# Performance work log

Measured on AMD Instinct MI355X. Metric: run time of the kernel, lower is better.

The kernel has to match this reference:

```python
import jax, jax.numpy as jnp
import numpy as np

# ---- reconstructed Constants (repo's Constants module is external) ----
DT, DX, DY, Z = 0.005, 0.01, 0.01, 1.0
_cf = np.array([-11.0 / 6.0, 3.0, -1.5, 1.0 / 3.0], np.float32)  # 3rd-order one-sided stencil
KF  = jnp.asarray(((DT / DX) * _cf).reshape(1, 4, 1, 1))           # H-field forward boundary kernel
KB  = jnp.asarray((-(DT / DX) * _cf[::-1]).reshape(1, 4, 1, 1))    # H-field backward boundary kernel
KEF = jnp.asarray(((DT / (Z * DY)) * _cf).reshape(1, 4, 1, 1))     # E-field forward boundary kernel
KEB = jnp.asarray((-(DT / (Z * DY)) * _cf[::-1]).reshape(1, 4, 1, 1))

PAD1   = ((0, 0), (2, 2), (2, 2), (0, 0))
PAD2   = ((0, 0), (0, 0), (1, 1), (0, 0))
PAD3   = ((0, 0), (1, 1), (0, 0), (0, 0))
PADY_F = ((0, 0), (0, 4), (1, 1), (0, 0))
PADY_B = ((0, 0), (4, 0), (1, 1), (0, 0))
PADX_F = ((0, 0), (1, 1), (0, 4), (0, 0))
PADX_B = ((0, 0), (1, 1), (4, 0), (0, 0))
PADEX_F = ((0, 0), (0, 0), (0, 2), (0, 0))
PADEX_B = ((0, 0), (0, 0), (2, 0), (0, 0))
PADEY_F = ((0, 0), (0, 2), (0, 0), (0, 0))
PADEY_B = ((0, 0), (2, 0), (0, 0), (0, 0))


def _conv(x, k):  # TF-style VALID cross-correlation, NHWC/HWIO
    return jax.lax.conv_general_dilated(x, k, (1, 1), 'VALID',
                                        dimension_numbers=('NHWC', 'HWIO', 'NHWC'))


def _T(k):  # swap the two spatial kernel dims (tf.transpose perm=[1,0,2,3])
    return jnp.transpose(k, (1, 0, 2, 3))


def _amper(E, Hx, Hy, f):
    S1 = (jnp.pad(DT / DX * _conv(Hy, _T(f)), PAD1)
          + jnp.pad(_conv(Hy, _T(KF)), PADY_F)
          + jnp.pad(_conv(Hy, _T(KB)), PADY_B))
    S2 = (jnp.pad(Z * DT / DY * _conv(Hx, f), PAD1)
          + jnp.pad(_conv(Hx, KF), PADX_F)
          + jnp.pad(_conv(Hx, KB), PADX_B))
    return E + S1 - S2


def _faraday(E, Hx, Hy, f):
    S3 = (DT / (Z * DY) * jnp.pad(_conv(E, f), PAD2)
          + jnp.pad(_conv(E, KEF), PADEX_F)[:, 1:-1, :, :]
          + jnp.pad(_conv(E, KEB), PADEX_B)[:, 1:-1, :, :])
    S4 = (DT / (Z * DX) * jnp.pad(_conv(E, _T(f)), PAD3)
          + jnp.pad(_conv(E, _T(KEF)), PADEY_F)[:, :, 1:-1, :]
          + jnp.pad(_conv(E, _T(KEB)), PADEY_B)[:, :, 1:-1, :])
    return Hx - S3, Hy + S4


def setup_inputs() -> dict:
    key = jax.random.key(0)
    k1, k2, k3 = jax.random.split(key, 3)
    B, P, Q = 8, 1024, 1024
    E = jax.random.normal(k1, (B, P, Q, 1), jnp.float32)
    Hx = jax.random.normal(k2, (B, P - 2, Q - 1, 1), jnp.float32)
    Hy = jax.random.normal(k3, (B, P - 1, Q - 2, 1), jnp.float32)
    filt = jnp.array([[1.0, -1.0, 1.0, 0.0],
                      [0.0, -1.0, 1.0, 0.0],
                      [1.0, -1.0, 1.0, 0.0]], jnp.float32).reshape(3, 4, 1, 1)
    return {'E': E, 'Hx': Hx, 'Hy': Hy, 'filt': filt}


def reference(E, Hx, Hy, filt):
    E_n = _amper(E, Hx, Hy, filt)
    Hx_n, Hy_n = _faraday(E_n, Hx, Hy, filt)
    E_m = _amper(E_n, Hx_n, Hy_n, filt)
    Hx_m, Hy_m = _faraday(E_m, Hx_n, Hy_n, filt)
    return (jnp.concatenate([E_n, E_m], 1),
            jnp.concatenate([Hx_n, Hx_m], 1),
            jnp.concatenate([Hy_n, Hy_m], 1))
```

## Files before the change

kernel.cpp:

```cpp
#include <hip/hip_runtime.h>


#define KF0 (-11.0f / 12.0f)
#define KF1 (1.5f)
#define KF2 (-0.75f)
#define KF3 (1.0f / 6.0f)
#define KB0 (-1.0f / 6.0f)
#define KB1 (0.75f)
#define KB2 (-1.5f)
#define KB3 (11.0f / 12.0f)

__global__ __launch_bounds__(256) void amper_k(
    const float* __restrict__ E, int sEb,
    const float* __restrict__ Hx, int sHxb,
    const float* __restrict__ Hy, int sHyb,
    float* __restrict__ Eo, int sEob)
{
    int x = blockIdx.x * 256 + threadIdx.x;
    int y = blockIdx.y;
    int b = blockIdx.z;
    const float* e  = E  + (size_t)b * sEb;
    const float* hx = Hx + (size_t)b * sHxb;
    const float* hy = Hy + (size_t)b * sHyb;

    float v = e[y * 1024 + x];

    if ((y >= 2) & (y < 1022) & (x >= 2) & (x < 1022)) {
        const float* r0 = hy + (y - 2) * 1022 + (x - 2);
        const float* r1 = r0 + 1022;
        const float* r2 = r1 + 1022;
        v += 0.5f * ((r0[0] + r0[2])
                     - (r1[0] + r1[1] + r1[2])
                     + (r2[0] + r2[1] + r2[2]));
        const float* q0 = hx + (y - 2) * 1023 + (x - 2);
        const float* q1 = q0 + 1023;
        const float* q2 = q1 + 1023;
        v -= 0.5f * ((q0[0] - q0[1] + q0[2])
                     + (-q1[1] + q1[2])
                     + (q2[0] - q2[1] + q2[2]));
    }
    bool cx = (x >= 1) & (x < 1023);
    if ((y < 1020) & cx) {
        const float* c = hy + y * 1022 + (x - 1);
        v += KF0 * c[0] + KF1 * c[1022] + KF2 * c[2044] + KF3 * c[3066];
    }
    if ((y >= 4) & cx) {
        const float* c = hy + (y - 4) * 1022 + (x - 1);
        v += KB0 * c[0] + KB1 * c[1022] + KB2 * c[2044] + KB3 * c[3066];
    }
    bool cy = (y >= 1) & (y < 1023);
    if (cy & (x < 1020)) {
        const float* r = hx + (y - 1) * 1023 + x;
        v -= KF0 * r[0] + KF1 * r[1] + KF2 * r[2] + KF3 * r[3];
    }
    if (cy & (x >= 4)) {
        const float* r = hx + (y - 1) * 1023 + (x - 4);
        v -= KB0 * r[0] + KB1 * r[1] + KB2 * r[2] + KB3 * r[3];
    }

    Eo[(size_t)b * sEob + y * 1024 + x] = v;
}

__global__ __launch_bounds__(256) void faraday_k(
    const float* __restrict__ E, int sEb,
    const float* __restrict__ Hx, int sHxb,
    const float* __restrict__ Hy, int sHyb,
    float* __restrict__ Hxo, int sHxob,
    float* __restrict__ Hyo, int sHyob)
{
    int x = blockIdx.x * 256 + threadIdx.x;
    int y = blockIdx.y;
    int b = blockIdx.z;
    const float* e = E + (size_t)b * sEb;

    if ((x < 1023) & (y < 1022)) {
        float v = (Hx + (size_t)b * sHxb)[y * 1023 + x];
        if ((x >= 1) & (x < 1022)) {
            const float* r0 = e + y * 1024 + (x - 1);
            const float* r1 = r0 + 1024;
            const float* r2 = r1 + 1024;
            v -= 0.5f * ((r0[0] - r0[1] + r0[2])
                         + (-r1[1] + r1[2])
                         + (r2[0] - r2[1] + r2[2]));
        }
        if (x < 1021) {
            const float* r = e + (y + 1) * 1024 + x;
            v -= KF0 * r[0] + KF1 * r[1] + KF2 * r[2] + KF3 * r[3];
        }
        if (x >= 2) {
            const float* r = e + (y + 1) * 1024 + (x - 2);
            v -= KB0 * r[0] + KB1 * r[1] + KB2 * r[2] + KB3 * r[3];
        }
        Hxo[(size_t)b * sHxob + y * 1023 + x] = v;
    }

    if (x < 1022) {
        float v = (Hy + (size_t)b * sHyb)[y * 1022 + x];
        if ((y >= 1) & (y < 1022)) {
            const float* r0 = e + (y - 1) * 1024 + x;
            const float* r1 = r0 + 1024;
            const float* r2 = r1 + 1024;
            v += 0.5f * ((r0[0] + r0[2])
                         - (r1[0] + r1[1] + r1[2])
                         + (r2[0] + r2[1] + r2[2]));
        }
        if (y < 1021) {
            const float* c = e + y * 1024 + (x + 1);
            v += KF0 * c[0] + KF1 * c[1024] + KF2 * c[2048] + KF3 * c[3072];
        }
        if (y >= 2) {
            const float* c = e + (y - 2) * 1024 + (x + 1);
            v += KB0 * c[0] + KB1 * c[1024] + KB2 * c[2048] + KB3 * c[3072];
        }
        Hyo[(size_t)b * sHyob + y * 1022 + x] = v;
    }
}

extern "C" void kernel_launch(void* const* d_in, const int* in_sizes, int n_in,
                              void* d_out, int out_size, void* d_ws, size_t ws_size,
                              hipStream_t stream)
{
    const float* E  = (const float*)d_in[0];
    const float* Hx = (const float*)d_in[1];
    const float* Hy = (const float*)d_in[2];

    float* out = (float*)d_out;
    float* Eo  = out;
    float* Hxo = out + 16777216;
    float* Hyo = Hxo + 16728096;

    const int sE = 1024 * 1024;
    const int sHx = 1022 * 1023;
    const int sHy = 1023 * 1022;
    const int sEo = 2 * 1024 * 1024;
    const int sHo = 2 * 1045506;

    dim3 blk(256, 1, 1);
    dim3 gA(4, 1024, 8);
    dim3 gF(4, 1023, 8);

    amper_k<<<gA, blk, 0, stream>>>(E, sE, Hx, sHx, Hy, sHy, Eo, sEo);
    faraday_k<<<gF, blk, 0, stream>>>(Eo, sEo, Hx, sHx, Hy, sHy,
                                      Hxo, sHo, Hyo, sHo);
    amper_k<<<gA, blk, 0, stream>>>(Eo, sEo, Hxo, sHo, Hyo, sHo,
                                    Eo + 1024 * 1024, sEo);
    faraday_k<<<gF, blk, 0, stream>>>(Eo + 1024 * 1024, sEo, Hxo, sHo, Hyo, sHo,
                                      Hxo + 1045506, sHo, Hyo + 1045506, sHo);
}
```

Measured before the change: 444.3 us.

## Compute four outputs per thread with vectorized row loads and register reuse

Each thread now computes four consecutive outputs. Interior points load their stencil rows as float4/float2 vectors and reuse overlapping values in registers, while boundary points fall back to scalar per-point helpers. Block indices are remapped so consecutive blocks interleave the batch index. This cuts the number of load instructions and redundant global reads, but many of the vector loads are unaligned (odd row strides such as 1022 and 1023) and the grid has a quarter as many threads.

```diff
diff --git a/kernel.cpp b/kernel.cpp
--- a/kernel.cpp
+++ b/kernel.cpp
@@ -10,21 +10,25 @@
 #define KB2 (-1.5f)
 #define KB3 (11.0f / 12.0f)
 
-__global__ __launch_bounds__(256) void amper_k(
-    const float* __restrict__ E, int sEb,
-    const float* __restrict__ Hx, int sHxb,
-    const float* __restrict__ Hy, int sHyb,
-    float* __restrict__ Eo, int sEob)
-{
-    int x = blockIdx.x * 256 + threadIdx.x;
-    int y = blockIdx.y;
-    int b = blockIdx.z;
-    const float* e  = E  + (size_t)b * sEb;
-    const float* hx = Hx + (size_t)b * sHxb;
-    const float* hy = Hy + (size_t)b * sHyb;
-
+typedef float f4 __attribute__((ext_vector_type(4)));
+typedef float f2 __attribute__((ext_vector_type(2)));
+
+__device__ __forceinline__ f4 ld4(const float* p) { f4 v; __builtin_memcpy(&v, p, 16); return v; }
+__device__ __forceinline__ f2 ld2(const float* p) { f2 v; __builtin_memcpy(&v, p, 8); return v; }
+__device__ __forceinline__ void st4(float* p, f4 v) { __builtin_memcpy(p, &v, 16); }
+
+#define LOAD6(dst, p) do { f4 _a = ld4(p); f2 _b = ld2((p) + 4); \
+    (dst)[0]=_a.x; (dst)[1]=_a.y; (dst)[2]=_a.z; (dst)[3]=_a.w; (dst)[4]=_b.x; (dst)[5]=_b.y; } while (0)
+#define LOAD4(dst, p) do { f4 _a = ld4(p); \
+    (dst)[0]=_a.x; (dst)[1]=_a.y; (dst)[2]=_a.z; (dst)[3]=_a.w; } while (0)
+
+
+__device__ __forceinline__ float amper_pt(const float* __restrict__ e,
+                                          const float* __restrict__ hx,
+                                          const float* __restrict__ hy,
+                                          int y, int x)
+{
     float v = e[y * 1024 + x];
-
     if ((y >= 2) & (y < 1022) & (x >= 2) & (x < 1022)) {
         const float* r0 = hy + (y - 2) * 1022 + (x - 2);
         const float* r1 = r0 + 1022;
@@ -57,9 +61,120 @@
         const float* r = hx + (y - 1) * 1023 + (x - 4);
         v -= KB0 * r[0] + KB1 * r[1] + KB2 * r[2] + KB3 * r[3];
     }
-
-    Eo[(size_t)b * sEob + y * 1024 + x] = v;
-}
+    return v;
+}
+
+__device__ __forceinline__ float far_hx_pt(const float* __restrict__ e,
+                                           const float* __restrict__ hxp,
+                                           int y, int x)
+{
+    float v = hxp[y * 1023 + x];
+    if ((x >= 1) & (x < 1022)) {
+        const float* r0 = e + y * 1024 + (x - 1);
+        const float* r1 = r0 + 1024;
+        const float* r2 = r1 + 1024;
+        v -= 0.5f * ((r0[0] - r0[1] + r0[2])
+                     + (-r1[1] + r1[2])
+                     + (r2[0] - r2[1] + r2[2]));
+    }
+    if (x < 1021) {
+        const float* r = e + (y + 1) * 1024 + x;
+        v -= KF0 * r[0] + KF1 * r[1] + KF2 * r[2] + KF3 * r[3];
+    }
+    if (x >= 2) {
+        const float* r = e + (y + 1) * 1024 + (x - 2);
+        v -= KB0 * r[0] + KB1 * r[1] + KB2 * r[2] + KB3 * r[3];
+    }
+    return v;
+}
+
+__device__ __forceinline__ float far_hy_pt(const float* __restrict__ e,
+                                           const float* __restrict__ hyp,
+                                           int y, int x)
+{
+    float v = hyp[y * 1022 + x];
+    if ((y >= 1) & (y < 1022)) {
+        const float* r0 = e + (y - 1) * 1024 + x;
+        const float* r1 = r0 + 1024;
+        const float* r2 = r1 + 1024;
+        v += 0.5f * ((r0[0] + r0[2])
+                     - (r1[0] + r1[1] + r1[2])
+                     + (r2[0] + r2[1] + r2[2]));
+    }
+    if (y < 1021) {
+        const float* c = e + y * 1024 + (x + 1);
+        v += KF0 * c[0] + KF1 * c[1024] + KF2 * c[2048] + KF3 * c[3072];
+    }
+    if (y >= 2) {
+        const float* c = e + (y - 2) * 1024 + (x + 1);
+        v += KB0 * c[0] + KB1 * c[1024] + KB2 * c[2048] + KB3 * c[3072];
+    }
+    return v;
+}
+
+
+__global__ __launch_bounds__(256) void amper_k(
+    const float* __restrict__ E, int sEb,
+    const float* __restrict__ Hx, int sHxb,
+    const float* __restrict__ Hy, int sHyb,
+    float* __restrict__ Eo, int sEob)
+{
+    int lin = blockIdx.y + (blockIdx.z << 10);
+    int b = lin & 7;
+    int y = lin >> 3;
+    int x0 = threadIdx.x << 2;
+
+    const float* e  = E  + (size_t)b * sEb;
+    const float* hx = Hx + (size_t)b * sHxb;
+    const float* hy = Hy + (size_t)b * sHyb;
+    float* eo = Eo + (size_t)b * sEob + y * 1024;
+
+    if ((y >= 4) & (y < 1020) & (x0 >= 4) & (x0 <= 1016)) {
+        float cA[6], cB[6], cC[6];
+        const float* hyr = hy + (y - 2) * 1022 + (x0 - 2);
+        LOAD6(cA, hyr);
+        LOAD6(cB, hyr + 1022);
+        LOAD6(cC, hyr + 2044);
+        float km4[4], km3[4], kp1[4], kp2[4], kp3[4];
+        const float* hyc = hy + (y - 4) * 1022 + (x0 - 1);
+        LOAD4(km4, hyc);
+        LOAD4(km3, hyc + 1022);
+        LOAD4(kp1, hyc + 5 * 1022);
+        LOAD4(kp2, hyc + 6 * 1022);
+        LOAD4(kp3, hyc + 7 * 1022);
+        float dA[6], dC[6], e12[12];
+        const float* hxr = hx + (y - 2) * 1023 + (x0 - 2);
+        LOAD6(dA, hxr);
+        LOAD6(dC, hxr + 2046);
+        const float* hxm = hx + (y - 1) * 1023 + (x0 - 4);
+        LOAD4(&e12[0], hxm);
+        LOAD4(&e12[4], hxm + 4);
+        LOAD4(&e12[8], hxm + 8);
+        f4 ev = ld4(e + y * 1024 + x0);
+        f4 o;
+        #pragma unroll
+        for (int j = 0; j < 4; ++j) {
+            float v = ev[j];
+            v += 0.5f * ((cA[j] + cA[j + 2])
+                         - (cB[j] + cB[j + 1] + cB[j + 2])
+                         + (cC[j] + cC[j + 1] + cC[j + 2]));
+            v -= 0.5f * ((dA[j] - dA[j + 1] + dA[j + 2])
+                         + (-e12[j + 3] + e12[j + 4])
+                         + (dC[j] - dC[j + 1] + dC[j + 2]));
+            v += KF0 * cC[j + 1] + KF1 * kp1[j] + KF2 * kp2[j] + KF3 * kp3[j];
+            v += KB0 * km4[j] + KB1 * km3[j] + KB2 * cA[j + 1] + KB3 * cB[j + 1];
+            v -= KF0 * e12[j + 4] + KF1 * e12[j + 5] + KF2 * e12[j + 6] + KF3 * e12[j + 7];
+            v -= KB0 * e12[j] + KB1 * e12[j + 1] + KB2 * e12[j + 2] + KB3 * e12[j + 3];
+            o[j] = v;
+        }
+        st4(eo + x0, o);
+    } else {
+        #pragma unroll
+        for (int j = 0; j < 4; ++j)
+            eo[x0 + j] = amper_pt(e, hx, hy, y, x0 + j);
+    }
+}
+
 
 __global__ __launch_bounds__(256) void faraday_k(
     const float* __restrict__ E, int sEb,
@@ -68,51 +183,79 @@
     float* __restrict__ Hxo, int sHxob,
     float* __restrict__ Hyo, int sHyob)
 {
-    int x = blockIdx.x * 256 + threadIdx.x;
-    int y = blockIdx.y;
-    int b = blockIdx.z;
+    int lin = blockIdx.y + 1023 * blockIdx.z;
+    int b = lin & 7;
+    int y = lin >> 3;
+    int x0 = threadIdx.x << 2;
+
     const float* e = E + (size_t)b * sEb;
-
-    if ((x < 1023) & (y < 1022)) {
-        float v = (Hx + (size_t)b * sHxb)[y * 1023 + x];
-        if ((x >= 1) & (x < 1022)) {
-            const float* r0 = e + y * 1024 + (x - 1);
-            const float* r1 = r0 + 1024;
-            const float* r2 = r1 + 1024;
-            v -= 0.5f * ((r0[0] - r0[1] + r0[2])
-                         + (-r1[1] + r1[2])
-                         + (r2[0] - r2[1] + r2[2]));
+    bool xfast = (x0 >= 4) & (x0 <= 1016);
+
+    if (y < 1022) {
+        const float* hxp = Hx + (size_t)b * sHxb;
+        float* hxo = Hxo + (size_t)b * sHxob + y * 1023;
+        if (xfast) {
+            float gA[6], gC[6], h9[9];
+            const float* er = e + y * 1024 + (x0 - 1);
+            LOAD6(gA, er);
+            LOAD6(gC, er + 2048);
+            const float* em = e + (y + 1) * 1024 + (x0 - 2);
+            LOAD4(&h9[0], em);
+            LOAD4(&h9[4], em + 4);
+            h9[8] = em[8];
+            f4 hv = ld4(hxp + y * 1023 + x0);
+            f4 o;
+            #pragma unroll
+            for (int j = 0; j < 4; ++j) {
+                float v = hv[j];
+                v -= 0.5f * ((gA[j] - gA[j + 1] + gA[j + 2])
+                             + (-h9[j + 2] + h9[j + 3])
+                             + (gC[j] - gC[j + 1] + gC[j + 2]));
+                v -= KF0 * h9[j + 2] + KF1 * h9[j + 3] + KF2 * h9[j + 4] + KF3 * h9[j + 5];
+                v -= KB0 * h9[j] + KB1 * h9[j + 1] + KB2 * h9[j + 2] + KB3 * h9[j + 3];
+                o[j] = v;
+            }
+            st4(hxo + x0, o);
+        } else {
+            for (int j = 0; j < 4; ++j) {
+                int x = x0 + j;
+                if (x < 1023) hxo[x] = far_hx_pt(e, hxp, y, x);
+            }
         }
-        if (x < 1021) {
-            const float* r = e + (y + 1) * 1024 + x;
-            v -= KF0 * r[0] + KF1 * r[1] + KF2 * r[2] + KF3 * r[3];
+    }
+
+    {
+        const float* hyp = Hy + (size_t)b * sHyb;
+        float* hyo = Hyo + (size_t)b * sHyob + y * 1022;
+        if (xfast & (y >= 2) & (y <= 1020)) {
+            float mA[6], mB[6], mC[6], nA[4], nD[4], nE[4];
+            const float* er = e + (y - 1) * 1024 + x0;
+            LOAD6(mA, er);
+            LOAD6(mB, er + 1024);
+            LOAD6(mC, er + 2048);
+            const float* en = e + (y - 2) * 1024 + (x0 + 1);
+            LOAD4(nA, en);
+            LOAD4(nD, en + 4 * 1024);
+            LOAD4(nE, en + 5 * 1024);
+            f4 hv = ld4(hyp + y * 1022 + x0);
+            f4 o;
+            #pragma unroll
+            for (int j = 0; j < 4; ++j) {
+                float v = hv[j];
+                v += 0.5f * ((mA[j] + mA[j + 2])
+                             - (mB[j] + mB[j + 1] + mB[j + 2])
+                             + (mC[j] + mC[j + 1] + mC[j + 2]));
+                v += KF0 * mB[j + 1] + KF1 * mC[j + 1] + KF2 * nD[j] + KF3 * nE[j];
+                v += KB0 * nA[j] + KB1 * mA[j + 1] + KB2 * mB[j + 1] + KB3 * mC[j + 1];
+                o[j] = v;
+            }
+            st4(hyo + x0, o);
+        } else {
+            for (int j = 0; j < 4; ++j) {
+                int x = x0 + j;
+                if (x < 1022) hyo[x] = far_hy_pt(e, hyp, y, x);
+            }
         }
-        if (x >= 2) {
-            const float* r = e + (y + 1) * 1024 + (x - 2);
-            v -= KB0 * r[0] + KB1 * r[1] + KB2 * r[2] + KB3 * r[3];
-        }
-        Hxo[(size_t)b * sHxob + y * 1023 + x] = v;
-    }
-
-    if (x < 1022) {
-        float v = (Hy + (size_t)b * sHyb)[y * 1022 + x];
-        if ((y >= 1) & (y < 1022)) {
-            const float* r0 = e + (y - 1) * 1024 + x;
-            const float* r1 = r0 + 1024;
-            const float* r2 = r1 + 1024;
-            v += 0.5f * ((r0[0] + r0[2])
-                         - (r1[0] + r1[1] + r1[2])
-                         + (r2[0] + r2[1] + r2[2]));
-        }
-        if (y < 1021) {
-            const float* c = e + y * 1024 + (x + 1);
-            v += KF0 * c[0] + KF1 * c[1024] + KF2 * c[2048] + KF3 * c[3072];
-        }
-        if (y >= 2) {
-            const float* c = e + (y - 2) * 1024 + (x + 1);
-            v += KB0 * c[0] + KB1 * c[1024] + KB2 * c[2048] + KB3 * c[3072];
-        }
-        Hyo[(size_t)b * sHyob + y * 1022 + x] = v;
     }
 }
 
@@ -136,8 +279,8 @@
     const int sHo = 2 * 1045506;
 
     dim3 blk(256, 1, 1);
-    dim3 gA(4, 1024, 8);
-    dim3 gF(4, 1023, 8);
+    dim3 gA(1, 1024, 8);
+    dim3 gF(1, 1023, 8);
 
     amper_k<<<gA, blk, 0, stream>>>(E, sE, Hx, sHx, Hy, sHy, Eo, sEo);
     faraday_k<<<gF, blk, 0, stream>>>(Eo, sEo, Hx, sHx, Hy, sHy,
```

Result: faster. 400.5 us (-9.9%).

## Fuse amper and faraday steps via LDS-staged E tile with halo recompute

Applied to the files above, without the earlier changes.

Merges the amper and faraday kernels into one kernel per half-step. Each block computes the updated E for an 8-row by 512-column tile plus halo rows and columns, keeps it in shared memory, and writes the interior to global memory. It then computes the Hx and Hy updates directly from shared memory. Interior work is vectorized to four elements per thread using 16-byte loads and stores. This removes the global write-then-reread of E between kernels and halves the launch count, at the cost of recomputing halo rows (13 rows per 8 output rows) and only 256 blocks per launch.

```diff
diff --git a/kernel.cpp b/kernel.cpp
--- a/kernel.cpp
+++ b/kernel.cpp
@@ -10,21 +10,20 @@
 #define KB2 (-1.5f)
 #define KB3 (11.0f / 12.0f)
 
-__global__ __launch_bounds__(256) void amper_k(
-    const float* __restrict__ E, int sEb,
-    const float* __restrict__ Hx, int sHxb,
-    const float* __restrict__ Hy, int sHyb,
-    float* __restrict__ Eo, int sEob)
-{
-    int x = blockIdx.x * 256 + threadIdx.x;
-    int y = blockIdx.y;
-    int b = blockIdx.z;
-    const float* e  = E  + (size_t)b * sEb;
-    const float* hx = Hx + (size_t)b * sHxb;
-    const float* hy = Hy + (size_t)b * sHyb;
-
+typedef float f4 __attribute__((ext_vector_type(4)));
+
+__device__ __forceinline__ f4 ld4(const float* p) { f4 v; __builtin_memcpy(&v, p, 16); return v; }
+__device__ __forceinline__ void st4(float* p, f4 v) { __builtin_memcpy(p, &v, 16); }
+
+#define LOAD6(dst, p) do { __builtin_memcpy(dst, p, 24); } while (0)
+#define LOAD4(dst, p) do { __builtin_memcpy(dst, p, 16); } while (0)
+
+__device__ __forceinline__ float amper_pt(const float* __restrict__ e,
+                                          const float* __restrict__ hx,
+                                          const float* __restrict__ hy,
+                                          int y, int x)
+{
     float v = e[y * 1024 + x];
-
     if ((y >= 2) & (y < 1022) & (x >= 2) & (x < 1022)) {
         const float* r0 = hy + (y - 2) * 1022 + (x - 2);
         const float* r1 = r0 + 1022;
@@ -57,62 +56,210 @@
         const float* r = hx + (y - 1) * 1023 + (x - 4);
         v -= KB0 * r[0] + KB1 * r[1] + KB2 * r[2] + KB3 * r[3];
     }
-
-    Eo[(size_t)b * sEob + y * 1024 + x] = v;
-}
-
-__global__ __launch_bounds__(256) void faraday_k(
+    return v;
+}
+
+#define EP 532
+#define ES_AT(r, c) eS[((r) - y0 + 2) * EP + ((c) - xb + 4)]
+
+__device__ __forceinline__ float far_hx_pt_lds(
+    const float* eS, const float* __restrict__ hxp,
+    int y0, int xb, int y, int x)
+{
+    float v = hxp[y * 1023 + x];
+    if ((x >= 1) & (x < 1022)) {
+        v -= 0.5f * ((ES_AT(y, x-1) - ES_AT(y, x) + ES_AT(y, x+1))
+                     + (-ES_AT(y+1, x) + ES_AT(y+1, x+1))
+                     + (ES_AT(y+2, x-1) - ES_AT(y+2, x) + ES_AT(y+2, x+1)));
+    }
+    if (x < 1021) {
+        v -= KF0 * ES_AT(y+1, x) + KF1 * ES_AT(y+1, x+1)
+           + KF2 * ES_AT(y+1, x+2) + KF3 * ES_AT(y+1, x+3);
+    }
+    if (x >= 2) {
+        v -= KB0 * ES_AT(y+1, x-2) + KB1 * ES_AT(y+1, x-1)
+           + KB2 * ES_AT(y+1, x) + KB3 * ES_AT(y+1, x+1);
+    }
+    return v;
+}
+
+__device__ __forceinline__ float far_hy_pt_lds(
+    const float* eS, const float* __restrict__ hyp,
+    int y0, int xb, int y, int x)
+{
+    float v = hyp[y * 1022 + x];
+    if ((y >= 1) & (y < 1022)) {
+        v += 0.5f * ((ES_AT(y-1, x) + ES_AT(y-1, x+2))
+                     - (ES_AT(y, x) + ES_AT(y, x+1) + ES_AT(y, x+2))
+                     + (ES_AT(y+1, x) + ES_AT(y+1, x+1) + ES_AT(y+1, x+2)));
+    }
+    if (y < 1021) {
+        v += KF0 * ES_AT(y, x+1) + KF1 * ES_AT(y+1, x+1)
+           + KF2 * ES_AT(y+2, x+1) + KF3 * ES_AT(y+3, x+1);
+    }
+    if (y >= 2) {
+        v += KB0 * ES_AT(y-2, x+1) + KB1 * ES_AT(y-1, x+1)
+           + KB2 * ES_AT(y, x+1) + KB3 * ES_AT(y+1, x+1);
+    }
+    return v;
+}
+
+__global__ __launch_bounds__(256) void fused_k(
     const float* __restrict__ E, int sEb,
     const float* __restrict__ Hx, int sHxb,
     const float* __restrict__ Hy, int sHyb,
+    float* __restrict__ Eo, int sEob,
     float* __restrict__ Hxo, int sHxob,
     float* __restrict__ Hyo, int sHyob)
 {
-    int x = blockIdx.x * 256 + threadIdx.x;
-    int y = blockIdx.y;
-    int b = blockIdx.z;
-    const float* e = E + (size_t)b * sEb;
-
-    if ((x < 1023) & (y < 1022)) {
-        float v = (Hx + (size_t)b * sHxb)[y * 1023 + x];
-        if ((x >= 1) & (x < 1022)) {
-            const float* r0 = e + y * 1024 + (x - 1);
-            const float* r1 = r0 + 1024;
-            const float* r2 = r1 + 1024;
-            v -= 0.5f * ((r0[0] - r0[1] + r0[2])
-                         + (-r1[1] + r1[2])
-                         + (r2[0] - r2[1] + r2[2]));
+    int xt = blockIdx.x;
+    int b  = blockIdx.y;
+    int s  = blockIdx.z;
+    int y0 = s << 3;
+    int xb = xt << 9;
+
+    const float* e  = E  + (size_t)b * sEb;
+    const float* hx = Hx + (size_t)b * sHxb;
+    const float* hy = Hy + (size_t)b * sHyb;
+    float* eo  = Eo  + (size_t)b * sEob;
+    float* hxo = Hxo + (size_t)b * sHxob;
+    float* hyo = Hyo + (size_t)b * sHyob;
+
+    __shared__ float eS[13 * EP];
+
+    int tid = threadIdx.x;
+
+    for (int idx = tid; idx < 13 * 132; idx += 256) {
+        int i = idx / 132, j = idx - i * 132;
+        int y  = y0 - 2 + i;
+        int c0 = xb - 4 + (j << 2);
+        if ((unsigned)y < 1024u) {
+            f4 o;
+            if ((y >= 4) & (y < 1020) & (c0 >= 4) & (c0 <= 1016)) {
+                float cA[6], cB[6], cC[6];
+                const float* hyr = hy + (y - 2) * 1022 + (c0 - 2);
+                LOAD6(cA, hyr);
+                LOAD6(cB, hyr + 1022);
+                LOAD6(cC, hyr + 2044);
+                float km4[4], km3[4], kp1[4], kp2[4], kp3[4];
+                const float* hyc = hy + (y - 4) * 1022 + (c0 - 1);
+                LOAD4(km4, hyc);
+                LOAD4(km3, hyc + 1022);
+                LOAD4(kp1, hyc + 5 * 1022);
+                LOAD4(kp2, hyc + 6 * 1022);
+                LOAD4(kp3, hyc + 7 * 1022);
+                float dA[6], dC[6], e12[12];
+                const float* hxr = hx + (y - 2) * 1023 + (c0 - 2);
+                LOAD6(dA, hxr);
+                LOAD6(dC, hxr + 2046);
+                const float* hxm = hx + (y - 1) * 1023 + (c0 - 4);
+                LOAD4(&e12[0], hxm);
+                LOAD4(&e12[4], hxm + 4);
+                LOAD4(&e12[8], hxm + 8);
+                f4 ev = ld4(e + y * 1024 + c0);
+                #pragma unroll
+                for (int k = 0; k < 4; ++k) {
+                    float v = ev[k];
+                    v += 0.5f * ((cA[k] + cA[k + 2])
+                                 - (cB[k] + cB[k + 1] + cB[k + 2])
+                                 + (cC[k] + cC[k + 1] + cC[k + 2]));
+                    v -= 0.5f * ((dA[k] - dA[k + 1] + dA[k + 2])
+                                 + (-e12[k + 3] + e12[k + 4])
+                                 + (dC[k] - dC[k + 1] + dC[k + 2]));
+                    v += KF0 * cC[k + 1] + KF1 * kp1[k] + KF2 * kp2[k] + KF3 * kp3[k];
+                    v += KB0 * km4[k] + KB1 * km3[k] + KB2 * cA[k + 1] + KB3 * cB[k + 1];
+                    v -= KF0 * e12[k + 4] + KF1 * e12[k + 5] + KF2 * e12[k + 6] + KF3 * e12[k + 7];
+                    v -= KB0 * e12[k] + KB1 * e12[k + 1] + KB2 * e12[k + 2] + KB3 * e12[k + 3];
+                    o[k] = v;
+                }
+            } else {
+                #pragma unroll
+                for (int k = 0; k < 4; ++k) {
+                    int x = c0 + k;
+                    o[k] = ((unsigned)x < 1024u) ? amper_pt(e, hx, hy, y, x) : 0.f;
+                }
+            }
+            st4(&eS[i * EP + (c0 - xb + 4)], o);
+            if ((y >= y0) & (y < y0 + 8) & (c0 >= xb) & (c0 <= xb + 508))
+                st4(eo + y * 1024 + c0, o);
         }
-        if (x < 1021) {
-            const float* r = e + (y + 1) * 1024 + x;
-            v -= KF0 * r[0] + KF1 * r[1] + KF2 * r[2] + KF3 * r[3];
+    }
+    __syncthreads();
+
+    int tx = tid & 127, ty = tid >> 7;
+    int c0 = xb + (tx << 2);
+    bool cfast = (c0 >= 4) & (c0 <= 1016);
+
+    #pragma unroll
+    for (int rr = 0; rr < 4; ++rr) {
+        int y = y0 + (ty << 2) + rr;
+
+        if (y < 1022) {
+            float* hxorow = hxo + y * 1023;
+            if (cfast) {
+                const float* er = &eS[(y - y0 + 2) * EP + (c0 - xb + 3)];
+                float gA[6], gC[6], h9[9];
+                LOAD6(gA, er);
+                LOAD6(gC, er + 2 * EP);
+                const float* em = &eS[(y - y0 + 3) * EP + (c0 - xb + 2)];
+                LOAD4(&h9[0], em);
+                LOAD4(&h9[4], em + 4);
+                h9[8] = em[8];
+                f4 hv = ld4(hx + y * 1023 + c0);
+                f4 o;
+                #pragma unroll
+                for (int k = 0; k < 4; ++k) {
+                    float v = hv[k];
+                    v -= 0.5f * ((gA[k] - gA[k + 1] + gA[k + 2])
+                                 + (-h9[k + 2] + h9[k + 3])
+                                 + (gC[k] - gC[k + 1] + gC[k + 2]));
+                    v -= KF0 * h9[k + 2] + KF1 * h9[k + 3] + KF2 * h9[k + 4] + KF3 * h9[k + 5];
+                    v -= KB0 * h9[k] + KB1 * h9[k + 1] + KB2 * h9[k + 2] + KB3 * h9[k + 3];
+                    o[k] = v;
+                }
+                st4(hxorow + c0, o);
+            } else {
+                #pragma unroll
+                for (int k = 0; k < 4; ++k) {
+                    int x = c0 + k;
+                    if (x < 1023) hxorow[x] = far_hx_pt_lds(eS, hx, y0, xb, y, x);
+                }
+            }
         }
-        if (x >= 2) {
-            const float* r = e + (y + 1) * 1024 + (x - 2);
-            v -= KB0 * r[0] + KB1 * r[1] + KB2 * r[2] + KB3 * r[3];
+
+        if (y < 1023) {
+            float* hyorow = hyo + y * 1022;
+            if (cfast & (y >= 2) & (y <= 1020)) {
+                const float* er = &eS[(y - y0 + 1) * EP + (c0 - xb + 4)];
+                float mA[6], mB[6], mC[6], nA[4], nD[4], nE[4];
+                LOAD6(mA, er);
+                LOAD6(mB, er + EP);
+                LOAD6(mC, er + 2 * EP);
+                const float* en = &eS[(y - y0) * EP + (c0 - xb + 5)];
+                LOAD4(nA, en);
+                LOAD4(nD, en + 4 * EP);
+                LOAD4(nE, en + 5 * EP);
+                f4 hv = ld4(hy + y * 1022 + c0);
+                f4 o;
+                #pragma unroll
+                for (int k = 0; k < 4; ++k) {
+                    float v = hv[k];
+                    v += 0.5f * ((mA[k] + mA[k + 2])
+                                 - (mB[k] + mB[k + 1] + mB[k + 2])
+                                 + (mC[k] + mC[k + 1] + mC[k + 2]));
+                    v += KF0 * mB[k + 1] + KF1 * mC[k + 1] + KF2 * nD[k] + KF3 * nE[k];
+                    v += KB0 * nA[k] + KB1 * mA[k + 1] + KB2 * mB[k + 1] + KB3 * mC[k + 1];
+                    o[k] = v;
+                }
+                st4(hyorow + c0, o);
+            } else {
+                #pragma unroll
+                for (int k = 0; k < 4; ++k) {
+                    int x = c0 + k;
+                    if (x < 1022) hyorow[x] = far_hy_pt_lds(eS, hy, y0, xb, y, x);
+                }
+            }
         }
-        Hxo[(size_t)b * sHxob + y * 1023 + x] = v;
-    }
-
-    if (x < 1022) {
-        float v = (Hy + (size_t)b * sHyb)[y * 1022 + x];
-        if ((y >= 1) & (y < 1022)) {
-            const float* r0 = e + (y - 1) * 1024 + x;
-            const float* r1 = r0 + 1024;
-            const float* r2 = r1 + 1024;
-            v += 0.5f * ((r0[0] + r0[2])
-                         - (r1[0] + r1[1] + r1[2])
-                         + (r2[0] + r2[1] + r2[2]));
-        }
-        if (y < 1021) {
-            const float* c = e + y * 1024 + (x + 1);
-            v += KF0 * c[0] + KF1 * c[1024] + KF2 * c[2048] + KF3 * c[3072];
-        }
-        if (y >= 2) {
-            const float* c = e + (y - 2) * 1024 + (x + 1);
-            v += KB0 * c[0] + KB1 * c[1024] + KB2 * c[2048] + KB3 * c[3072];
-        }
-        Hyo[(size_t)b * sHyob + y * 1022 + x] = v;
     }
 }
 
@@ -129,21 +276,18 @@
     float* Hxo = out + 16777216;
     float* Hyo = Hxo + 16728096;
 
-    const int sE = 1024 * 1024;
+    const int sE  = 1024 * 1024;
     const int sHx = 1022 * 1023;
     const int sHy = 1023 * 1022;
     const int sEo = 2 * 1024 * 1024;
     const int sHo = 2 * 1045506;
 
     dim3 blk(256, 1, 1);
-    dim3 gA(4, 1024, 8);
-    dim3 gF(4, 1023, 8);
-
-    amper_k<<<gA, blk, 0, stream>>>(E, sE, Hx, sHx, Hy, sHy, Eo, sEo);
-    faraday_k<<<gF, blk, 0, stream>>>(Eo, sEo, Hx, sHx, Hy, sHy,
-                                      Hxo, sHo, Hyo, sHo);
-    amper_k<<<gA, blk, 0, stream>>>(Eo, sEo, Hxo, sHo, Hyo, sHo,
-                                    Eo + 1024 * 1024, sEo);
-    faraday_k<<<gF, blk, 0, stream>>>(Eo + 1024 * 1024, sEo, Hxo, sHo, Hyo, sHo,
-                                      Hxo + 1045506, sHo, Hyo + 1045506, sHo);
-}
+    dim3 g(2, 8, 128);
+
+    fused_k<<<g, blk, 0, stream>>>(E, sE, Hx, sHx, Hy, sHy,
+                                   Eo, sEo, Hxo, sHo, Hyo, sHo);
+    fused_k<<<g, blk, 0, stream>>>(Eo, sEo, Hxo, sHo, Hyo, sHo,
+                                   Eo + 1024 * 1024, sEo,
+                                   Hxo + 1045506, sHo, Hyo + 1045506, sHo);
+}
```

Result: slower. 516.3 us (+16.2%).

## Register-tile stencils: 4 columns x 8 rows per thread with rolling row windows

Applied to the files above, without the earlier changes.

Both stencil kernels are restructured so each thread produces 4 adjacent columns over 8 consecutive rows. Input rows are held in a rolling register window, so each loaded row serves several output rows. Loads and stores become wider vector accesses, and edge columns go through a scalar fallback path. This cuts redundant global and L2 loads and per-element index arithmetic, at the cost of far fewer blocks (1024 per launch), higher register pressure, and possibly misaligned vector accesses on the 1023- and 1022-wide rows.

```diff
diff --git a/kernel.cpp b/kernel.cpp
--- a/kernel.cpp
+++ b/kernel.cpp
@@ -10,21 +10,18 @@
 #define KB2 (-1.5f)
 #define KB3 (11.0f / 12.0f)
 
-__global__ __launch_bounds__(256) void amper_k(
-    const float* __restrict__ E, int sEb,
-    const float* __restrict__ Hx, int sHxb,
-    const float* __restrict__ Hy, int sHyb,
-    float* __restrict__ Eo, int sEob)
-{
-    int x = blockIdx.x * 256 + threadIdx.x;
-    int y = blockIdx.y;
-    int b = blockIdx.z;
-    const float* e  = E  + (size_t)b * sEb;
-    const float* hx = Hx + (size_t)b * sHxb;
-    const float* hy = Hy + (size_t)b * sHyb;
-
+typedef float f4 __attribute__((ext_vector_type(4)));
+
+__device__ __forceinline__ f4 ld4(const float* p) { f4 v; __builtin_memcpy(&v, p, 16); return v; }
+__device__ __forceinline__ void st4(float* p, f4 v) { __builtin_memcpy(p, &v, 16); }
+
+
+__device__ __forceinline__ float amper_pt(const float* __restrict__ e,
+                                          const float* __restrict__ hx,
+                                          const float* __restrict__ hy,
+                                          int y, int x)
+{
     float v = e[y * 1024 + x];
-
     if ((y >= 2) & (y < 1022) & (x >= 2) & (x < 1022)) {
         const float* r0 = hy + (y - 2) * 1022 + (x - 2);
         const float* r1 = r0 + 1022;
@@ -57,62 +54,286 @@
         const float* r = hx + (y - 1) * 1023 + (x - 4);
         v -= KB0 * r[0] + KB1 * r[1] + KB2 * r[2] + KB3 * r[3];
     }
-
-    Eo[(size_t)b * sEob + y * 1024 + x] = v;
-}
-
-__global__ __launch_bounds__(256) void faraday_k(
+    return v;
+}
+
+__device__ __forceinline__ float far_hx_pt(const float* __restrict__ e,
+                                           const float* __restrict__ hxp,
+                                           int y, int x)
+{
+    float v = hxp[y * 1023 + x];
+    if ((x >= 1) & (x < 1022)) {
+        const float* r0 = e + y * 1024 + (x - 1);
+        const float* r1 = r0 + 1024;
+        const float* r2 = r1 + 1024;
+        v -= 0.5f * ((r0[0] - r0[1] + r0[2])
+                     + (-r1[1] + r1[2])
+                     + (r2[0] - r2[1] + r2[2]));
+    }
+    if (x < 1021) {
+        const float* r = e + (y + 1) * 1024 + x;
+        v -= KF0 * r[0] + KF1 * r[1] + KF2 * r[2] + KF3 * r[3];
+    }
+    if (x >= 2) {
+        const float* r = e + (y + 1) * 1024 + (x - 2);
+        v -= KB0 * r[0] + KB1 * r[1] + KB2 * r[2] + KB3 * r[3];
+    }
+    return v;
+}
+
+__device__ __forceinline__ float far_hy_pt(const float* __restrict__ e,
+                                           const float* __restrict__ hyp,
+                                           int y, int x)
+{
+    float v = hyp[y * 1022 + x];
+    if ((y >= 1) & (y < 1022)) {
+        const float* r0 = e + (y - 1) * 1024 + x;
+        const float* r1 = r0 + 1024;
+        const float* r2 = r1 + 1024;
+        v += 0.5f * ((r0[0] + r0[2])
+                     - (r1[0] + r1[1] + r1[2])
+                     + (r2[0] + r2[1] + r2[2]));
+    }
+    if (y < 1021) {
+        const float* c = e + y * 1024 + (x + 1);
+        v += KF0 * c[0] + KF1 * c[1024] + KF2 * c[2048] + KF3 * c[3072];
+    }
+    if (y >= 2) {
+        const float* c = e + (y - 2) * 1024 + (x + 1);
+        v += KB0 * c[0] + KB1 * c[1024] + KB2 * c[2048] + KB3 * c[3072];
+    }
+    return v;
+}
+
+
+__global__ __launch_bounds__(256) void amper_m(
+    const float* __restrict__ E, int sEb,
+    const float* __restrict__ Hx, int sHxb,
+    const float* __restrict__ Hy, int sHyb,
+    float* __restrict__ Eo, int sEob)
+{
+    int b  = blockIdx.x;
+    int y0 = blockIdx.y << 3;
+    int tid = threadIdx.x;
+    int x0 = tid << 2;
+
+    const float* e  = E  + (size_t)b * sEb;
+    const float* hx = Hx + (size_t)b * sHxb;
+    const float* hy = Hy + (size_t)b * sHyb;
+    float* eo = Eo + (size_t)b * sEob;
+
+    bool fast = (x0 >= 4) & (x0 <= 1016);
+
+    if (fast) {
+        float W[8][6];
+        float X[4][12];
+
+        #pragma unroll
+        for (int t = -4; t <= 2; ++t) {
+            int gr = y0 + t;
+            float* w = W[(t + 8) & 7];
+            if ((unsigned)gr < 1023u) {
+                __builtin_memcpy(w, hy + gr * 1022 + (x0 - 2), 24);
+            } else {
+                #pragma unroll
+                for (int k = 0; k < 6; ++k) w[k] = 0.f;
+            }
+        }
+        #pragma unroll
+        for (int t = -2; t <= -1; ++t) {
+            int gr = y0 + t;
+            float* w = X[(t + 8) & 3];
+            if ((unsigned)gr < 1022u) {
+                __builtin_memcpy(w, hx + gr * 1023 + (x0 - 4), 48);
+            } else {
+                #pragma unroll
+                for (int k = 0; k < 12; ++k) w[k] = 0.f;
+            }
+        }
+
+        #define WY(d) (W[(i + (d) + 8) & 7])
+        #define XX(d) (X[(i + (d) + 8) & 3])
+
+        #pragma unroll
+        for (int i = 0; i < 8; ++i) {
+            int y = y0 + i;
+            {
+                int gr = y + 3;
+                float* w = W[(i + 3) & 7];
+                if (gr <= 1022) {
+                    __builtin_memcpy(w, hy + gr * 1022 + (x0 - 2), 24);
+                } else {
+                    #pragma unroll
+                    for (int k = 0; k < 6; ++k) w[k] = 0.f;
+                }
+            }
+            {
+                float* w = X[(i + 8) & 3];
+                if (y <= 1021) {
+                    __builtin_memcpy(w, hx + y * 1023 + (x0 - 4), 48);
+                } else {
+                    #pragma unroll
+                    for (int k = 0; k < 12; ++k) w[k] = 0.f;
+                }
+            }
+            f4 ev = ld4(e + y * 1024 + x0);
+            f4 o;
+            bool gin = (y >= 2) & (y < 1022);
+            bool gf  = (y < 1020);
+            bool gb  = (y >= 4);
+            bool gc  = (y >= 1) & (y < 1023);
+            #pragma unroll
+            for (int j = 0; j < 4; ++j) {
+                float v = ev[j];
+                if (gin) {
+                    v += 0.5f * ((WY(-2)[j] + WY(-2)[j + 2])
+                                 - (WY(-1)[j] + WY(-1)[j + 1] + WY(-1)[j + 2])
+                                 + (WY(0)[j] + WY(0)[j + 1] + WY(0)[j + 2]));
+                    v -= 0.5f * ((XX(-2)[j + 2] - XX(-2)[j + 3] + XX(-2)[j + 4])
+                                 + (-XX(-1)[j + 3] + XX(-1)[j + 4])
+                                 + (XX(0)[j + 2] - XX(0)[j + 3] + XX(0)[j + 4]));
+                }
+                if (gf)
+                    v += KF0 * WY(0)[j + 1] + KF1 * WY(1)[j + 1]
+                       + KF2 * WY(2)[j + 1] + KF3 * WY(3)[j + 1];
+                if (gb)
+                    v += KB0 * WY(-4)[j + 1] + KB1 * WY(-3)[j + 1]
+                       + KB2 * WY(-2)[j + 1] + KB3 * WY(-1)[j + 1];
+                if (gc) {
+                    v -= KF0 * XX(-1)[j + 4] + KF1 * XX(-1)[j + 5]
+                       + KF2 * XX(-1)[j + 6] + KF3 * XX(-1)[j + 7];
+                    v -= KB0 * XX(-1)[j] + KB1 * XX(-1)[j + 1]
+                       + KB2 * XX(-1)[j + 2] + KB3 * XX(-1)[j + 3];
+                }
+                o[j] = v;
+            }
+            st4(eo + y * 1024 + x0, o);
+        }
+        #undef WY
+        #undef XX
+    } else {
+        for (int i = 0; i < 8; ++i) {
+            int y = y0 + i;
+            #pragma unroll
+            for (int k = 0; k < 4; ++k)
+                eo[y * 1024 + x0 + k] = amper_pt(e, hx, hy, y, x0 + k);
+        }
+    }
+}
+
+
+__global__ __launch_bounds__(256) void faraday_m(
     const float* __restrict__ E, int sEb,
     const float* __restrict__ Hx, int sHxb,
     const float* __restrict__ Hy, int sHyb,
     float* __restrict__ Hxo, int sHxob,
     float* __restrict__ Hyo, int sHyob)
 {
-    int x = blockIdx.x * 256 + threadIdx.x;
-    int y = blockIdx.y;
-    int b = blockIdx.z;
-    const float* e = E + (size_t)b * sEb;
-
-    if ((x < 1023) & (y < 1022)) {
-        float v = (Hx + (size_t)b * sHxb)[y * 1023 + x];
-        if ((x >= 1) & (x < 1022)) {
-            const float* r0 = e + y * 1024 + (x - 1);
-            const float* r1 = r0 + 1024;
-            const float* r2 = r1 + 1024;
-            v -= 0.5f * ((r0[0] - r0[1] + r0[2])
-                         + (-r1[1] + r1[2])
-                         + (r2[0] - r2[1] + r2[2]));
-        }
-        if (x < 1021) {
-            const float* r = e + (y + 1) * 1024 + x;
-            v -= KF0 * r[0] + KF1 * r[1] + KF2 * r[2] + KF3 * r[3];
-        }
-        if (x >= 2) {
-            const float* r = e + (y + 1) * 1024 + (x - 2);
-            v -= KB0 * r[0] + KB1 * r[1] + KB2 * r[2] + KB3 * r[3];
-        }
-        Hxo[(size_t)b * sHxob + y * 1023 + x] = v;
-    }
-
-    if (x < 1022) {
-        float v = (Hy + (size_t)b * sHyb)[y * 1022 + x];
-        if ((y >= 1) & (y < 1022)) {
-            const float* r0 = e + (y - 1) * 1024 + x;
-            const float* r1 = r0 + 1024;
-            const float* r2 = r1 + 1024;
-            v += 0.5f * ((r0[0] + r0[2])
-                         - (r1[0] + r1[1] + r1[2])
-                         + (r2[0] + r2[1] + r2[2]));
-        }
-        if (y < 1021) {
-            const float* c = e + y * 1024 + (x + 1);
-            v += KF0 * c[0] + KF1 * c[1024] + KF2 * c[2048] + KF3 * c[3072];
-        }
-        if (y >= 2) {
-            const float* c = e + (y - 2) * 1024 + (x + 1);
-            v += KB0 * c[0] + KB1 * c[1024] + KB2 * c[2048] + KB3 * c[3072];
-        }
-        Hyo[(size_t)b * sHyob + y * 1022 + x] = v;
+    int b  = blockIdx.x;
+    int y0 = blockIdx.y << 3;
+    int tid = threadIdx.x;
+    int x0 = tid << 2;
+
+    const float* e   = E  + (size_t)b * sEb;
+    const float* hxp = Hx + (size_t)b * sHxb;
+    const float* hyp = Hy + (size_t)b * sHyb;
+    float* hxo = Hxo + (size_t)b * sHxob;
+    float* hyo = Hyo + (size_t)b * sHyob;
+
+    bool fast = (x0 >= 4) & (x0 <= 1016);
+
+    if (fast) {
+        float Ew[8][12];
+
+        #pragma unroll
+        for (int t = -2; t <= 2; ++t) {
+            int gr = y0 + t;
+            float* w = Ew[(t + 8) & 7];
+            if ((unsigned)gr < 1024u) {
+                __builtin_memcpy(w, e + gr * 1024 + (x0 - 4), 48);
+            } else {
+                #pragma unroll
+                for (int k = 0; k < 12; ++k) w[k] = 0.f;
+            }
+        }
+
+        #define EWD(d) (Ew[(i + (d) + 8) & 7])
+
+        #pragma unroll
+        for (int i = 0; i < 8; ++i) {
+            int y = y0 + i;
+            {
+                int gr = y + 3;
+                float* w = Ew[(i + 3) & 7];
+                if (gr <= 1023) {
+                    __builtin_memcpy(w, e + gr * 1024 + (x0 - 4), 48);
+                } else {
+                    #pragma unroll
+                    for (int k = 0; k < 12; ++k) w[k] = 0.f;
+                }
+            }
+
+            if (y < 1022) {
+                f4 hv = ld4(hxp + y * 1023 + x0);
+                f4 o;
+                #pragma unroll
+                for (int j = 0; j < 4; ++j) {
+                    float v = hv[j];
+                    v -= 0.5f * ((EWD(0)[j + 3] - EWD(0)[j + 4] + EWD(0)[j + 5])
+                                 + (-EWD(1)[j + 4] + EWD(1)[j + 5])
+                                 + (EWD(2)[j + 3] - EWD(2)[j + 4] + EWD(2)[j + 5]));
+                    v -= KF0 * EWD(1)[j + 4] + KF1 * EWD(1)[j + 5]
+                       + KF2 * EWD(1)[j + 6] + KF3 * EWD(1)[j + 7];
+                    v -= KB0 * EWD(1)[j + 2] + KB1 * EWD(1)[j + 3]
+                       + KB2 * EWD(1)[j + 4] + KB3 * EWD(1)[j + 5];
+                    o[j] = v;
+                }
+                st4(hxo + y * 1023 + x0, o);
+            }
+
+            if (y < 1023) {
+                f4 hv = ld4(hyp + y * 1022 + x0);
+                f4 o;
+                bool ga = (y >= 1) & (y < 1022);
+                bool gf = (y < 1021);
+                bool gb = (y >= 2);
+                #pragma unroll
+                for (int j = 0; j < 4; ++j) {
+                    float v = hv[j];
+                    if (ga)
+                        v += 0.5f * ((EWD(-1)[j + 4] + EWD(-1)[j + 6])
+                                     - (EWD(0)[j + 4] + EWD(0)[j + 5] + EWD(0)[j + 6])
+                                     + (EWD(1)[j + 4] + EWD(1)[j + 5] + EWD(1)[j + 6]));
+                    if (gf)
+                        v += KF0 * EWD(0)[j + 5] + KF1 * EWD(1)[j + 5]
+                           + KF2 * EWD(2)[j + 5] + KF3 * EWD(3)[j + 5];
+                    if (gb)
+                        v += KB0 * EWD(-2)[j + 5] + KB1 * EWD(-1)[j + 5]
+                           + KB2 * EWD(0)[j + 5] + KB3 * EWD(1)[j + 5];
+                    o[j] = v;
+                }
+                st4(hyo + y * 1022 + x0, o);
+            }
+        }
+        #undef EWD
+    } else {
+        for (int i = 0; i < 8; ++i) {
+            int y = y0 + i;
+            if (y < 1022) {
+                #pragma unroll
+                for (int k = 0; k < 4; ++k) {
+                    int x = x0 + k;
+                    if (x < 1023) hxo[y * 1023 + x] = far_hx_pt(e, hxp, y, x);
+                }
+            }
+            if (y < 1023) {
+                #pragma unroll
+                for (int k = 0; k < 4; ++k) {
+                    int x = x0 + k;
+                    if (x < 1022) hyo[y * 1022 + x] = far_hy_pt(e, hyp, y, x);
+                }
+            }
+        }
     }
 }
 
@@ -129,21 +350,20 @@
     float* Hxo = out + 16777216;
     float* Hyo = Hxo + 16728096;
 
-    const int sE = 1024 * 1024;
+    const int sE  = 1024 * 1024;
     const int sHx = 1022 * 1023;
     const int sHy = 1023 * 1022;
     const int sEo = 2 * 1024 * 1024;
     const int sHo = 2 * 1045506;
 
     dim3 blk(256, 1, 1);
-    dim3 gA(4, 1024, 8);
-    dim3 gF(4, 1023, 8);
-
-    amper_k<<<gA, blk, 0, stream>>>(E, sE, Hx, sHx, Hy, sHy, Eo, sEo);
-    faraday_k<<<gF, blk, 0, stream>>>(Eo, sEo, Hx, sHx, Hy, sHy,
-                                      Hxo, sHo, Hyo, sHo);
-    amper_k<<<gA, blk, 0, stream>>>(Eo, sEo, Hxo, sHo, Hyo, sHo,
-                                    Eo + 1024 * 1024, sEo);
-    faraday_k<<<gF, blk, 0, stream>>>(Eo + 1024 * 1024, sEo, Hxo, sHo, Hyo, sHo,
-                                      Hxo + 1045506, sHo, Hyo + 1045506, sHo);
-}
+    dim3 g(8, 128, 1);
+
+    amper_m<<<g, blk, 0, stream>>>(E, sE, Hx, sHx, Hy, sHy, Eo, sEo);
+    faraday_m<<<g, blk, 0, stream>>>(Eo, sEo, Hx, sHx, Hy, sHy,
+                                     Hxo, sHo, Hyo, sHo);
+    amper_m<<<g, blk, 0, stream>>>(Eo, sEo, Hxo, sHo, Hyo, sHo,
+                                   Eo + 1024 * 1024, sEo);
+    faraday_m<<<g, blk, 0, stream>>>(Eo + 1024 * 1024, sEo, Hxo, sHo, Hyo, sHo,
+                                     Hxo + 1045506, sHo, Hyo + 1045506, sHo);
+}
```

Result: slower. 554.1 us (+24.7%).
